# Kernel tuning notes

Hardware: AMD Instinct MI355X
Metric: run time of the kernel (lower is better)

The kernel has to match this reference:

```python
import jax, jax.numpy as jnp
import numpy as np

B, S, D, H = 8, 1500, 1024, 16
HD = D // H
DFF = 4 * D
EPS = 1e-5


def _xavier(key, shape):
    fan_in, fan_out = shape[1], shape[0]
    limit = float(np.sqrt(6.0 / (fan_in + fan_out)))
    return jax.random.uniform(key, shape, jnp.float32, -limit, limit)


def setup_inputs() -> dict:
    key = jax.random.key(0)
    ks = jax.random.split(key, 8)
    return {
        "hidden_states": jax.random.normal(ks[0], (B, S, D), jnp.float32),
        "Wq": _xavier(ks[1], (D, D)),
        "Wk": _xavier(ks[2], (D, D)),
        "Wv": _xavier(ks[3], (D, D)),
        "Wo": _xavier(ks[4], (D, D)),
        "W1": _xavier(ks[5], (DFF, D)),
        "b1": jnp.zeros((DFF,), jnp.float32),
        "W2": _xavier(ks[6], (D, DFF)),
        "b2": jnp.zeros((D,), jnp.float32),
        "ln1_g": jnp.ones((D,), jnp.float32),
        "ln1_b": jnp.zeros((D,), jnp.float32),
        "ln2_g": jnp.ones((D,), jnp.float32),
        "ln2_b": jnp.zeros((D,), jnp.float32),
    }


def _layernorm(x, g, b):
    mu = jnp.mean(x, axis=-1, keepdims=True)
    var = jnp.mean(jnp.square(x - mu), axis=-1, keepdims=True)
    return (x - mu) * jax.lax.rsqrt(var + EPS) * g + b


def reference(hidden_states, Wq, Wk, Wv, Wo, W1, b1, W2, b2, ln1_g, ln1_b, ln2_g, ln2_b):
    x = hidden_states
    residual = x
    h = _layernorm(x, ln1_g, ln1_b)
    # torch Linear: y = h @ W.T ; reshape to heads
    q = (h @ Wq.T).reshape(B, S, H, HD).transpose(0, 2, 1, 3) * (HD ** -0.5)
    k = (h @ Wk.T).reshape(B, S, H, HD).transpose(0, 2, 1, 3)
    v = (h @ Wv.T).reshape(B, S, H, HD).transpose(0, 2, 1, 3)
    scores = jnp.einsum('bhqd,bhkd->bhqk', q, k)
    attn = jax.nn.softmax(scores.astype(jnp.float32), axis=-1).astype(h.dtype)
    ctx = jnp.einsum('bhqk,bhkd->bhqd', attn, v)
    ctx = ctx.transpose(0, 2, 1, 3).reshape(B, S, D)
    x = residual + ctx @ Wo.T
    residual = x
    h = _layernorm(x, ln2_g, ln2_b)
    ffn = jax.nn.gelu(h @ W1.T + b1, approximate=False) @ W2.T + b2
    return residual + ffn
```

## Files before the change

kernel.cpp:

```cpp
#include <hip/hip_runtime.h>
#include <hip/hip_bf16.h>
#include <cstdint>
#include <cstddef>

#define B_    8
#define S_    1500
#define D_    1024
#define H_    16
#define HD_   64
#define DFF_  4096
#define M_    12000
#define VTS_  1536

typedef __bf16 bf16;
typedef __attribute__((ext_vector_type(8))) __bf16 bf16x8;
typedef __attribute__((ext_vector_type(4))) float f32x4;

#define MFMA16(a, b, c) __builtin_amdgcn_mfma_f32_16x16x32_bf16((a), (b), (c), 0, 0, 0)

#define BAR()   do { __builtin_amdgcn_s_barrier(); __builtin_amdgcn_sched_barrier(0); } while (0)

static __device__ __forceinline__ void gload16(const void* g, void* l) {
  __builtin_amdgcn_global_load_lds(
      (const __attribute__((address_space(1))) void*)(uintptr_t)g,
      (__attribute__((address_space(3))) void*)(uintptr_t)l, 16, 0, 0);
}

static __device__ __forceinline__ unsigned short f2bu(float v) {
  bf16 h = (bf16)v;
  union { bf16 h; unsigned short u; } c;
  c.h = h;
  return c.u;
}

static constexpr size_t HSZ      = (size_t)M_ * D_ * 2;
static constexpr size_t H_OFF    = 0;
static constexpr size_t WQ_OFF   = H_OFF + HSZ;
static constexpr size_t WK_OFF   = WQ_OFF + (size_t)D_ * D_ * 2;
static constexpr size_t WV_OFF   = WK_OFF + (size_t)D_ * D_ * 2;
static constexpr size_t WO_OFF   = WV_OFF + (size_t)D_ * D_ * 2;
static constexpr size_t Q_OFF    = WO_OFF + (size_t)D_ * D_ * 2;
static constexpr size_t K_OFF    = Q_OFF + HSZ;
static constexpr size_t VT_OFF   = K_OFF + HSZ;
static constexpr size_t W1_OFF   = VT_OFF + (size_t)128 * 64 * VTS_ * 2;
static constexpr size_t W2_OFF   = W1_OFF + (size_t)DFF_ * D_ * 2;
static constexpr size_t WS_BASE  = W2_OFF + (size_t)DFF_ * D_ * 2;
static constexpr size_t H2B_OFF  = WS_BASE;
static constexpr size_t NEED_BIG = WS_BASE + HSZ;
static constexpr size_t H2F_OFF  = VT_OFF;
static constexpr size_t ACT_OFF  = 0;

__launch_bounds__(256)
__global__ void cvt_bf16(const float* __restrict__ src, bf16* __restrict__ dst, int n) {
  int i = (blockIdx.x * 256 + threadIdx.x) * 4;
  if (i < n) {
    float4 f = *(const float4*)(src + i);
    dst[i + 0] = (bf16)f.x;
    dst[i + 1] = (bf16)f.y;
    dst[i + 2] = (bf16)f.z;
    dst[i + 3] = (bf16)f.w;
  }
}

__launch_bounds__(256)
__global__ void ln_fused(const float* __restrict__ x, const float* __restrict__ g,
                         const float* __restrict__ bb, bf16* __restrict__ out) {
  const int row = blockIdx.x;
  const int t = threadIdx.x;
  const float4 xv = *(const float4*)(x + (size_t)row * D_ + t * 4);
  float s  = xv.x + xv.y + xv.z + xv.w;
  float s2 = xv.x * xv.x + xv.y * xv.y + xv.z * xv.z + xv.w * xv.w;
#pragma unroll
  for (int m = 32; m >= 1; m >>= 1) {
    s  += __shfl_xor(s, m);
    s2 += __shfl_xor(s2, m);
  }
  __shared__ float red[8];
  const int w = t >> 6;
  if ((t & 63) == 0) { red[w] = s; red[4 + w] = s2; }
  __syncthreads();
  s  = red[0] + red[1] + red[2] + red[3];
  s2 = red[4] + red[5] + red[6] + red[7];
  const float mu  = s * (1.0f / D_);
  const float var = s2 * (1.0f / D_) - mu * mu;
  const float rs  = rsqrtf(var + 1e-5f);
  const float4 gv = *(const float4*)(g + t * 4);
  const float4 bv = *(const float4*)(bb + t * 4);
  bf16* o = out + (size_t)row * D_ + t * 4;
  o[0] = (bf16)((xv.x - mu) * rs * gv.x + bv.x);
  o[1] = (bf16)((xv.y - mu) * rs * gv.y + bv.y);
  o[2] = (bf16)((xv.z - mu) * rs * gv.z + bv.z);
  o[3] = (bf16)((xv.w - mu) * rs * gv.w + bv.w);
}

template <int EPI>
__launch_bounds__(512, 2)
__global__ void gemm256(const bf16* __restrict__ A, const bf16* __restrict__ Bw,
                        int M, int N, int K,
                        bf16* __restrict__ outB, float* outF,
                        const float* __restrict__ bias, const float* resid,
                        bf16* __restrict__ outQ, bf16* __restrict__ outK2,
                        bf16* __restrict__ outV) {
  __shared__ bf16 a_lds[4][256 * 32];
  __shared__ bf16 b_lds[4][256 * 32];

  const int t = threadIdx.x;
  const int lane = t & 63, wid = t >> 6;
  const int wm = wid >> 2, wn = wid & 3;
  const int l15 = lane & 15, hi = lane >> 4;
  const int mrow0 = blockIdx.x * 256;
  const int ncol0 = blockIdx.y * 256;

  const int pc = hi ^ ((l15 >> 1) & 3);

  const int s0 = t, s1 = 512 + t;
  const int ar0 = s0 >> 2, ar1 = s1 >> 2;
  const int ac0 = ((s0 & 3) ^ ((ar0 >> 1) & 3)) * 8;
  const int ac1 = ((s1 & 3) ^ ((ar1 >> 1) & 3)) * 8;
  int ga0 = mrow0 + ar0; ga0 = ga0 < M ? ga0 : M - 1;
  int ga1 = mrow0 + ar1; ga1 = ga1 < M ? ga1 : M - 1;
  const bf16* a0 = A + (size_t)ga0 * K + ac0;
  const bf16* a1 = A + (size_t)ga1 * K + ac1;
  const bf16* b0 = Bw + (size_t)(ncol0 + ar0) * K + ac0;
  const bf16* b1 = Bw + (size_t)(ncol0 + ar1) * K + ac1;

  f32x4 acc[8][4] = {};

  const int NT = K >> 5;

#pragma unroll
  for (int pt = 0; pt < 3; ++pt) {
    const int kp = pt << 5;
    gload16(a0 + kp, (char*)&a_lds[pt][0] + s0 * 16);
    gload16(a1 + kp, (char*)&a_lds[pt][0] + s1 * 16);
    gload16(b0 + kp, (char*)&b_lds[pt][0] + s0 * 16);
    gload16(b1 + kp, (char*)&b_lds[pt][0] + s1 * 16);
  }
  asm volatile("s_waitcnt vmcnt(8)" ::: "memory");
  BAR();

  int buf = 0;
  for (int tt = 0; tt < NT; ++tt) {
    const bf16* al = &a_lds[buf][0];
    const bf16* bl = &b_lds[buf][0];
    const bool st3 = (tt + 3) < NT;
    const int nb = (tt + 3) & 3;
    const int k3 = (tt + 3) << 5;

    if (st3) {
      gload16(a0 + k3, (char*)&a_lds[nb][0] + s0 * 16);
      gload16(a1 + k3, (char*)&a_lds[nb][0] + s1 * 16);
      gload16(b0 + k3, (char*)&b_lds[nb][0] + s0 * 16);
      gload16(b1 + k3, (char*)&b_lds[nb][0] + s1 * 16);
    }

    bf16x8 bf_[4], af_[8];
#pragma unroll
    for (int n = 0; n < 4; ++n)
      bf_[n] = *(const bf16x8*)&bl[(wn * 64 + n * 16 + l15) * 32 + pc * 8];
#pragma unroll
    for (int m = 0; m < 8; ++m)
      af_[m] = *(const bf16x8*)&al[(wm * 128 + m * 16 + l15) * 32 + pc * 8];

    __builtin_amdgcn_s_setprio(1);
#pragma unroll
    for (int m = 0; m < 8; ++m)
#pragma unroll
      for (int n = 0; n < 4; ++n)
        acc[m][n] = MFMA16(af_[m], bf_[n], acc[m][n]);
    __builtin_amdgcn_s_setprio(0);

    if (st3)                  asm volatile("s_waitcnt vmcnt(8)" ::: "memory");
    else if ((tt + 2) < NT)   asm volatile("s_waitcnt vmcnt(4)" ::: "memory");
    else                      asm volatile("s_waitcnt vmcnt(0)" ::: "memory");
    BAR();
    buf = (buf + 1) & 3;
  }

  const int r0 = hi * 4;

  if constexpr (EPI == 5) {
    const int mm = blockIdx.y >> 2;
    const int nloc0 = (blockIdx.y & 3) * 256;
    if (mm == 2) {
#pragma unroll
      for (int m = 0; m < 8; ++m) {
        int row0 = mrow0 + wm * 128 + m * 16 + r0;
        if (row0 < M) {
          int bb2 = row0 / 1500;
          int s = row0 - bb2 * 1500;
#pragma unroll
          for (int n = 0; n < 4; ++n) {
            int f = nloc0 + wn * 64 + n * 16 + l15;
            size_t a = ((size_t)(bb2 * 16 + (f >> 6)) * 64 + (f & 63)) * VTS_ + s;
            ushort4 pk;
            pk.x = f2bu(acc[m][n][0]);
            pk.y = f2bu(acc[m][n][1]);
            pk.z = f2bu(acc[m][n][2]);
            pk.w = f2bu(acc[m][n][3]);
            *reinterpret_cast<ushort4*>((unsigned short*)outV + a) = pk;
          }
        }
      }
    } else {
      bf16* dst = (mm == 0) ? outQ : outK2;
      const float sc = (mm == 0) ? 0.18033688011112042f : 1.0f;
#pragma unroll
      for (int m = 0; m < 8; ++m) {
#pragma unroll
        for (int n = 0; n < 4; ++n) {
          int col = nloc0 + wn * 64 + n * 16 + l15;
#pragma unroll
          for (int r = 0; r < 4; ++r) {
            int row = mrow0 + wm * 128 + m * 16 + r0 + r;
            if (row < M) dst[(size_t)row * D_ + col] = (bf16)(acc[m][n][r] * sc);
          }
        }
      }
    }
    return;
  }

#pragma unroll
  for (int m = 0; m < 8; ++m) {
#pragma unroll
    for (int n = 0; n < 4; ++n) {
      int col = ncol0 + wn * 64 + n * 16 + l15;
#pragma unroll
      for (int r = 0; r < 4; ++r) {
        int row = mrow0 + wm * 128 + m * 16 + r0 + r;
        if (row < M) {
          float v = acc[m][n][r];
          if constexpr (EPI == 2) {
            float xg = v + bias[col];
            v = 0.5f * xg * (1.0f + erff(xg * 0.70710678118654752f));
            outB[(size_t)row * N + col] = (bf16)v;
          }
          if constexpr (EPI == 3) {
            v += resid[(size_t)row * N + col];
            if (bias) v += bias[col];
            outF[(size_t)row * N + col] = v;
          }
        }
      }
    }
  }
}

template <int EPI>
__launch_bounds__(256)
__global__ void gemm_bt(const bf16* __restrict__ A, const bf16* __restrict__ Bw,
                        int M, int N, int K,
                        bf16* __restrict__ outB, float* outF,
                        const float* __restrict__ bias, const float* resid,
                        float scale) {
  __shared__ bf16 a_lds[128 * 64];
  __shared__ bf16 b_lds[128 * 64];
  const int t = threadIdx.x;
  const int lane = t & 63, wid = t >> 6;
  const int wr = wid >> 1, wc = wid & 1;
  const int mrow0 = blockIdx.x * 128;
  const int ncol0 = blockIdx.y * 128;
  const int l15 = lane & 15;
  const int khi = (lane >> 4) << 3;

  f32x4 acc[4][4] = {};

  for (int k0 = 0; k0 < K; k0 += 64) {
#pragma unroll
    for (int i = 0; i < 4; ++i) {
      int idx = i * 2048 + t * 8;
      int row = idx >> 6, col = idx & 63;
      int gr = mrow0 + row;
      gr = gr < M ? gr : M - 1;
      gload16(A + (size_t)gr * K + (k0 + col), (char*)a_lds + idx * 2);
    }
#pragma unroll
    for (int i = 0; i < 4; ++i) {
      int idx = i * 2048 + t * 8;
      int row = idx >> 6, col = idx & 63;
      gload16(Bw + (size_t)(ncol0 + row) * K + (k0 + col), (char*)b_lds + idx * 2);
    }
    __syncthreads();
#pragma unroll
    for (int kk = 0; kk < 2; ++kk) {
      bf16x8 af[4], bfv[4];
#pragma unroll
      for (int m = 0; m < 4; ++m)
        af[m] = *(const bf16x8*)&a_lds[(wr * 64 + m * 16 + l15) * 64 + kk * 32 + khi];
#pragma unroll
      for (int n = 0; n < 4; ++n)
        bfv[n] = *(const bf16x8*)&b_lds[(wc * 64 + n * 16 + l15) * 64 + kk * 32 + khi];
#pragma unroll
      for (int m = 0; m < 4; ++m)
#pragma unroll
        for (int n = 0; n < 4; ++n)
          acc[m][n] = MFMA16(af[m], bfv[n], acc[m][n]);
    }
    __syncthreads();
  }

  const int r0 = (lane >> 4) << 2;
#pragma unroll
  for (int m = 0; m < 4; ++m) {
#pragma unroll
    for (int n = 0; n < 4; ++n) {
      int col = ncol0 + wc * 64 + n * 16 + l15;
#pragma unroll
      for (int r = 0; r < 4; ++r) {
        int row = mrow0 + wr * 64 + m * 16 + r0 + r;
        if (row < M) {
          float v = acc[m][n][r];
          if constexpr (EPI == 2) {
            float xg = v + bias[col];
            v = 0.5f * xg * (1.0f + erff(xg * 0.70710678118654752f));
          }
          if constexpr (EPI == 3) {
            v += resid[(size_t)row * N + col];
            if (bias) v += bias[col];
            outF[(size_t)row * N + col] = v;
          } else {
            outB[(size_t)row * N + col] = (bf16)v;
          }
        }
      }
    }
  }
}

__launch_bounds__(256, 4)
__global__ void attn_fwd6(const bf16* __restrict__ q, const bf16* __restrict__ kg,
                          const bf16* __restrict__ vt, bf16* __restrict__ cx) {
  __shared__ bf16 k_lds[2][64 * 64];
  __shared__ bf16 v_lds[2][64 * 64];
  __shared__ bf16 p_lds[4][16 * 64];

  const int t = threadIdx.x;
  const int lane = t & 63, w = t >> 6;
  const int L = blockIdx.x;
  const int wu = (L & 7) * 384 + (L >> 3);
  const int bh = wu / 24;
  const int qt = wu - bh * 24;
  const int l15 = lane & 15;
  const int hi = lane >> 4;
  const int khi = hi << 3;

  const size_t hoff = ((size_t)(bh >> 4) * S_) * D_ + (size_t)(bh & 15) * HD_;
  const bf16* qh = q + hoff;
  const bf16* kh = kg + hoff;
  const bf16* vh = vt + (size_t)bh * (64 * VTS_);

  const int st_r0 = t >> 3;
  const int st_c  = t & 7;

  int qr = qt * 64 + w * 16 + l15;
  int qrc = qr < S_ ? qr : S_ - 1;
  const bf16x8 qf0 = *(const bf16x8*)(qh + (size_t)qrc * D_ + khi);
  const bf16x8 qf1 = *(const bf16x8*)(qh + (size_t)qrc * D_ + 32 + khi);

  f32x4 oacc[4] = {};
  float mrun[4], lrun[4];
#pragma unroll
  for (int r = 0; r < 4; ++r) { mrun[r] = -1e30f; lrun[r] = 0.f; }

  bf16* pw = &p_lds[w][0];
  const int NT = (S_ + 63) / 64;
  const float THR = 11.5415605f;

#pragma unroll
  for (int i = 0; i < 2; ++i) {
    int row = i * 32 + st_r0;
    int sc = st_c ^ (row & 7);
    int key = row < S_ ? row : S_ - 1;
    gload16(kh + (size_t)key * D_ + sc * 8, (char*)&k_lds[0][0] + (i * 2048 + t * 8) * 2);
    gload16(vh + (size_t)row * VTS_ + sc * 8, (char*)&v_lds[0][0] + (i * 2048 + t * 8) * 2);
  }
  __syncthreads();

  int buf = 0;
  for (int kt = 0; kt < NT; ++kt) {
    if (kt + 1 < NT) {
      int kb = (kt + 1) * 64;
#pragma unroll
      for (int i = 0; i < 2; ++i) {
        int row = i * 32 + st_r0;
        int sc = st_c ^ (row & 7);
        int key = kb + row;
        key = key < S_ ? key : S_ - 1;
        gload16(kh + (size_t)key * D_ + sc * 8,
                (char*)&k_lds[buf ^ 1][0] + (i * 2048 + t * 8) * 2);
        gload16(vh + (size_t)row * VTS_ + kb + sc * 8,
                (char*)&v_lds[buf ^ 1][0] + (i * 2048 + t * 8) * 2);
      }
    }

    float pv[4][4];
    __builtin_amdgcn_s_setprio(1);
#pragma unroll
    for (int nb = 0; nb < 4; ++nb) {
      int krow = nb * 16 + l15;
      f32x4 z = {};
      z = MFMA16(qf0, *(const bf16x8*)&k_lds[buf][krow * 64 + ((hi ^ (l15 & 7)) << 3)], z);
      z = MFMA16(qf1, *(const bf16x8*)&k_lds[buf][krow * 64 + (((4 + hi) ^ (l15 & 7)) << 3)], z);
#pragma unroll
      for (int r = 0; r < 4; ++r) pv[nb][r] = z[r];
    }
    __builtin_amdgcn_s_setprio(0);

    if (kt == NT - 1) {
#pragma unroll
      for (int nb = 0; nb < 4; ++nb) {
        bool cvld = (kt * 64 + nb * 16 + l15) < S_;
#pragma unroll
        for (int r = 0; r < 4; ++r) pv[nb][r] = cvld ? pv[nb][r] : -1e30f;
      }
    }

    float lmax[4];
    bool ok = true;
#pragma unroll
    for (int r = 0; r < 4; ++r) {
      lmax[r] = fmaxf(fmaxf(pv[0][r], pv[1][r]), fmaxf(pv[2][r], pv[3][r]));
      ok = ok && (lmax[r] <= mrun[r] + THR);
    }
    if (!__all(ok)) {
#pragma unroll
      for (int r = 0; r < 4; ++r) {
        float mx = lmax[r];
        mx = fmaxf(mx, __shfl_xor(mx, 1));
        mx = fmaxf(mx, __shfl_xor(mx, 2));
        mx = fmaxf(mx, __shfl_xor(mx, 4));
        mx = fmaxf(mx, __shfl_xor(mx, 8));
        float mnew = fmaxf(mrun[r], mx);
        float corr = exp2f(mrun[r] - mnew);
        lrun[r] *= corr;
        mrun[r] = mnew;
#pragma unroll
        for (int db = 0; db < 4; ++db) oacc[db][r] *= corr;
      }
    }

#pragma unroll
    for (int r = 0; r < 4; ++r) {
      float p0 = exp2f(pv[0][r] - mrun[r]);
      float p1 = exp2f(pv[1][r] - mrun[r]);
      float p2 = exp2f(pv[2][r] - mrun[r]);
      float p3 = exp2f(pv[3][r] - mrun[r]);
      pv[0][r] = p0; pv[1][r] = p1; pv[2][r] = p2; pv[3][r] = p3;
      lrun[r] += (p0 + p1) + (p2 + p3);
    }

#pragma unroll
    for (int nb = 0; nb < 4; ++nb) {
#pragma unroll
      for (int r = 0; r < 4; ++r) {
        int prow = hi * 4 + r;
        int pcol = (nb * 16 + l15) ^ ((prow & 7) << 3);
        pw[prow * 64 + pcol] = (bf16)pv[nb][r];
      }
    }

    __builtin_amdgcn_s_setprio(1);
#pragma unroll
    for (int kk = 0; kk < 2; ++kk) {
      bf16x8 pf = *(const bf16x8*)&pw[l15 * 64 + (((kk * 4 + hi) ^ (l15 & 7)) << 3)];
#pragma unroll
      for (int db = 0; db < 4; ++db) {
        int vrow = db * 16 + l15;
        bf16x8 vf = *(const bf16x8*)&v_lds[buf][vrow * 64 + (((kk * 4 + hi) ^ (l15 & 7)) << 3)];
        oacc[db] = MFMA16(pf, vf, oacc[db]);
      }
    }
    __builtin_amdgcn_s_setprio(0);

    __syncthreads();
    buf ^= 1;
  }

#pragma unroll
  for (int r = 0; r < 4; ++r) {
    float ps = lrun[r];
    ps += __shfl_xor(ps, 1);
    ps += __shfl_xor(ps, 2);
    ps += __shfl_xor(ps, 4);
    ps += __shfl_xor(ps, 8);
    int qrow = qt * 64 + w * 16 + hi * 4 + r;
    if (qrow < S_) {
      float inv = 1.0f / ps;
#pragma unroll
      for (int db = 0; db < 4; ++db)
        cx[hoff + (size_t)qrow * D_ + db * 16 + l15] = (bf16)(oacc[db][r] * inv);
    }
  }
}

extern "C" void kernel_launch(void* const* d_in, const int* in_sizes, int n_in,
                              void* d_out, int out_size, void* d_ws, size_t ws_size,
                              hipStream_t stream) {
  const float* x   = (const float*)d_in[0];
  const float* Wq  = (const float*)d_in[1];
  const float* Wk  = (const float*)d_in[2];
  const float* Wv  = (const float*)d_in[3];
  const float* Wo  = (const float*)d_in[4];
  const float* W1  = (const float*)d_in[5];
  const float* b1  = (const float*)d_in[6];
  const float* W2  = (const float*)d_in[7];
  const float* b2  = (const float*)d_in[8];
  const float* g1  = (const float*)d_in[9];
  const float* be1 = (const float*)d_in[10];
  const float* g2  = (const float*)d_in[11];
  const float* be2 = (const float*)d_in[12];
  float* out = (float*)d_out;

  char* ws = (char*)d_ws;
  bf16* h_b   = (bf16*)(ws + H_OFF);
  bf16* wq_b  = (bf16*)(ws + WQ_OFF);
  bf16* wk_b  = (bf16*)(ws + WK_OFF);
  bf16* wv_b  = (bf16*)(ws + WV_OFF);
  bf16* wo_b  = (bf16*)(ws + WO_OFF);
  bf16* w1_b  = (bf16*)(ws + W1_OFF);
  bf16* w2_b  = (bf16*)(ws + W2_OFF);
  bf16* q_b   = (bf16*)(ws + Q_OFF);
  bf16* k_b   = (bf16*)(ws + K_OFF);
  bf16* vt_b  = (bf16*)(ws + VT_OFF);
  bf16* act_b = (bf16*)(ws + ACT_OFF);
  bf16* ctx_b = h_b;

  const bool big = ws_size >= NEED_BIG;
  bf16* h2_b = (bf16*)(ws + (big ? H2B_OFF : H2F_OFF));

  cvt_bf16<<<(D_ * D_) / 1024, 256, 0, stream>>>(Wq, wq_b, D_ * D_);
  cvt_bf16<<<(D_ * D_) / 1024, 256, 0, stream>>>(Wk, wk_b, D_ * D_);
  cvt_bf16<<<(D_ * D_) / 1024, 256, 0, stream>>>(Wv, wv_b, D_ * D_);
  cvt_bf16<<<(D_ * D_) / 1024, 256, 0, stream>>>(Wo, wo_b, D_ * D_);
  cvt_bf16<<<(DFF_ * D_) / 1024, 256, 0, stream>>>(W1, w1_b, DFF_ * D_);
  cvt_bf16<<<(DFF_ * D_) / 1024, 256, 0, stream>>>(W2, w2_b, DFF_ * D_);

  ln_fused<<<M_, 256, 0, stream>>>(x, g1, be1, h_b);

  gemm256<5><<<dim3((M_ + 255) / 256, 12), 512, 0, stream>>>(
      h_b, wq_b, M_, 3072, D_, nullptr, nullptr, nullptr, nullptr, q_b, k_b, vt_b);

  attn_fwd6<<<3072, 256, 0, stream>>>(q_b, k_b, vt_b, ctx_b);

  gemm256<3><<<dim3((M_ + 255) / 256, 4), 512, 0, stream>>>(
      ctx_b, wo_b, M_, D_, D_, nullptr, out, nullptr, x, nullptr, nullptr, nullptr);

  ln_fused<<<M_, 256, 0, stream>>>(out, g2, be2, h2_b);

  if (big) {
    gemm256<2><<<dim3((M_ + 255) / 256, DFF_ / 256), 512, 0, stream>>>(
        h2_b, w1_b, M_, DFF_, D_, act_b, nullptr, b1, nullptr,
        nullptr, nullptr, nullptr);
    gemm256<3><<<dim3((M_ + 255) / 256, D_ / 256), 512, 0, stream>>>(
        act_b, w2_b, M_, D_, DFF_, nullptr, out, b2, out,
        nullptr, nullptr, nullptr);
  } else {
    for (int c = 0; c < 3; ++c) {
      int r0c = c * 4000;
      int nr = 4000;
      gemm256<2><<<dim3((nr + 255) / 256, DFF_ / 256), 512, 0, stream>>>(
          h2_b + (size_t)r0c * D_, w1_b, nr, DFF_, D_, act_b, nullptr, b1, nullptr,
          nullptr, nullptr, nullptr);
      gemm_bt<3><<<dim3((nr + 127) / 128, D_ / 128), 256, 0, stream>>>(
          act_b, w2_b, nr, D_, DFF_, nullptr, out + (size_t)r0c * D_, b2,
          out + (size_t)r0c * D_, 0.f);
    }
  }
}
```

Baseline: 728.6 us.

## Restructure 256x256 GEMM to 1024 threads, K=64 double-buffered LDS tiles

The GEMM kernel goes from 512 to 1024 threads per block. Each of the 16 waves now computes a 64x64 sub-tile instead of 128x64, and the K-step grows from 32 to 64. The 4-stage pipeline with 32-wide K slices is replaced by a 2-stage double buffer with a new XOR swizzle and __syncthreads barriers. This cuts per-thread accumulator registers and adds waves to hide latency, at the cost of a shallower prefetch depth and a full barrier every K step.

```diff
diff --git a/kernel.cpp b/kernel.cpp
--- a/kernel.cpp
+++ b/kernel.cpp
@@ -17,8 +17,6 @@
 typedef __attribute__((ext_vector_type(4))) float f32x4;
 
 #define MFMA16(a, b, c) __builtin_amdgcn_mfma_f32_16x16x32_bf16((a), (b), (c), 0, 0, 0)
-
-#define BAR()   do { __builtin_amdgcn_s_barrier(); __builtin_amdgcn_sched_barrier(0); } while (0)
 
 static __device__ __forceinline__ void gload16(const void* g, void* l) {
   __builtin_amdgcn_global_load_lds(
@@ -94,87 +92,83 @@
 }
 
 template <int EPI>
-__launch_bounds__(512, 2)
+__launch_bounds__(1024, 4)
 __global__ void gemm256(const bf16* __restrict__ A, const bf16* __restrict__ Bw,
                         int M, int N, int K,
                         bf16* __restrict__ outB, float* outF,
                         const float* __restrict__ bias, const float* resid,
                         bf16* __restrict__ outQ, bf16* __restrict__ outK2,
                         bf16* __restrict__ outV) {
-  __shared__ bf16 a_lds[4][256 * 32];
-  __shared__ bf16 b_lds[4][256 * 32];
+  __shared__ bf16 a_lds[2][256 * 64];
+  __shared__ bf16 b_lds[2][256 * 64];
 
   const int t = threadIdx.x;
   const int lane = t & 63, wid = t >> 6;
   const int wm = wid >> 2, wn = wid & 3;
   const int l15 = lane & 15, hi = lane >> 4;
+  const int l7 = l15 & 7;
   const int mrow0 = blockIdx.x * 256;
   const int ncol0 = blockIdx.y * 256;
 
-  const int pc = hi ^ ((l15 >> 1) & 3);
-
-  const int s0 = t, s1 = 512 + t;
-  const int ar0 = s0 >> 2, ar1 = s1 >> 2;
-  const int ac0 = ((s0 & 3) ^ ((ar0 >> 1) & 3)) * 8;
-  const int ac1 = ((s1 & 3) ^ ((ar1 >> 1) & 3)) * 8;
-  int ga0 = mrow0 + ar0; ga0 = ga0 < M ? ga0 : M - 1;
-  int ga1 = mrow0 + ar1; ga1 = ga1 < M ? ga1 : M - 1;
-  const bf16* a0 = A + (size_t)ga0 * K + ac0;
-  const bf16* a1 = A + (size_t)ga1 * K + ac1;
-  const bf16* b0 = Bw + (size_t)(ncol0 + ar0) * K + ac0;
-  const bf16* b1 = Bw + (size_t)(ncol0 + ar1) * K + ac1;
-
-  f32x4 acc[8][4] = {};
-
-  const int NT = K >> 5;
-
-#pragma unroll
-  for (int pt = 0; pt < 3; ++pt) {
-    const int kp = pt << 5;
-    gload16(a0 + kp, (char*)&a_lds[pt][0] + s0 * 16);
-    gload16(a1 + kp, (char*)&a_lds[pt][0] + s1 * 16);
-    gload16(b0 + kp, (char*)&b_lds[pt][0] + s0 * 16);
-    gload16(b1 + kp, (char*)&b_lds[pt][0] + s1 * 16);
-  }
-  asm volatile("s_waitcnt vmcnt(8)" ::: "memory");
-  BAR();
+  const int rl = t >> 3;
+  const int sc8 = ((t & 7) ^ (rl & 7)) << 3;
+  unsigned offA[2], offB[2];
+#pragma unroll
+  for (int j = 0; j < 2; ++j) {
+    int gr = mrow0 + j * 128 + rl; gr = gr < M ? gr : M - 1;
+    offA[j] = (unsigned)gr * (unsigned)K + (unsigned)sc8;
+    offB[j] = (unsigned)(ncol0 + j * 128 + rl) * (unsigned)K + (unsigned)sc8;
+  }
+
+  f32x4 acc[4][4] = {};
+
+  const int NT = K >> 6;
+
+  {
+    char* ad = (char*)&a_lds[0][0];
+    char* bd = (char*)&b_lds[0][0];
+    gload16(A + offA[0], ad + t * 16);
+    gload16(A + offA[1], ad + 16384 + t * 16);
+    gload16(Bw + offB[0], bd + t * 16);
+    gload16(Bw + offB[1], bd + 16384 + t * 16);
+  }
+  __syncthreads();
 
   int buf = 0;
   for (int tt = 0; tt < NT; ++tt) {
+    if (tt + 1 < NT) {
+      const unsigned k1 = (unsigned)(tt + 1) << 6;
+      char* ad = (char*)&a_lds[buf ^ 1][0];
+      char* bd = (char*)&b_lds[buf ^ 1][0];
+      gload16(A + offA[0] + k1, ad + t * 16);
+      gload16(A + offA[1] + k1, ad + 16384 + t * 16);
+      gload16(Bw + offB[0] + k1, bd + t * 16);
+      gload16(Bw + offB[1] + k1, bd + 16384 + t * 16);
+    }
+
     const bf16* al = &a_lds[buf][0];
     const bf16* bl = &b_lds[buf][0];
-    const bool st3 = (tt + 3) < NT;
-    const int nb = (tt + 3) & 3;
-    const int k3 = (tt + 3) << 5;
-
-    if (st3) {
-      gload16(a0 + k3, (char*)&a_lds[nb][0] + s0 * 16);
-      gload16(a1 + k3, (char*)&a_lds[nb][0] + s1 * 16);
-      gload16(b0 + k3, (char*)&b_lds[nb][0] + s0 * 16);
-      gload16(b1 + k3, (char*)&b_lds[nb][0] + s1 * 16);
-    }
-
-    bf16x8 bf_[4], af_[8];
-#pragma unroll
-    for (int n = 0; n < 4; ++n)
-      bf_[n] = *(const bf16x8*)&bl[(wn * 64 + n * 16 + l15) * 32 + pc * 8];
-#pragma unroll
-    for (int m = 0; m < 8; ++m)
-      af_[m] = *(const bf16x8*)&al[(wm * 128 + m * 16 + l15) * 32 + pc * 8];
-
-    __builtin_amdgcn_s_setprio(1);
-#pragma unroll
-    for (int m = 0; m < 8; ++m)
+#pragma unroll
+    for (int kk = 0; kk < 2; ++kk) {
+      bf16x8 af_[4], bf_[4];
+      const int cc = ((kk * 4 + hi) ^ l7) << 3;
+#pragma unroll
+      for (int m = 0; m < 4; ++m)
+        af_[m] = *(const bf16x8*)&al[(wm * 64 + m * 16 + l15) * 64 + cc];
 #pragma unroll
       for (int n = 0; n < 4; ++n)
-        acc[m][n] = MFMA16(af_[m], bf_[n], acc[m][n]);
-    __builtin_amdgcn_s_setprio(0);
-
-    if (st3)                  asm volatile("s_waitcnt vmcnt(8)" ::: "memory");
-    else if ((tt + 2) < NT)   asm volatile("s_waitcnt vmcnt(4)" ::: "memory");
-    else                      asm volatile("s_waitcnt vmcnt(0)" ::: "memory");
-    BAR();
-    buf = (buf + 1) & 3;
+        bf_[n] = *(const bf16x8*)&bl[(wn * 64 + n * 16 + l15) * 64 + cc];
+      __builtin_amdgcn_s_setprio(1);
+#pragma unroll
+      for (int m = 0; m < 4; ++m)
+#pragma unroll
+        for (int n = 0; n < 4; ++n)
+          acc[m][n] = MFMA16(af_[m], bf_[n], acc[m][n]);
+      __builtin_amdgcn_s_setprio(0);
+    }
+
+    __syncthreads();
+    buf ^= 1;
   }
 
   const int r0 = hi * 4;
@@ -184,8 +178,8 @@
     const int nloc0 = (blockIdx.y & 3) * 256;
     if (mm == 2) {
 #pragma unroll
-      for (int m = 0; m < 8; ++m) {
-        int row0 = mrow0 + wm * 128 + m * 16 + r0;
+      for (int m = 0; m < 4; ++m) {
+        int row0 = mrow0 + wm * 64 + m * 16 + r0;
         if (row0 < M) {
           int bb2 = row0 / 1500;
           int s = row0 - bb2 * 1500;
@@ -206,13 +200,13 @@
       bf16* dst = (mm == 0) ? outQ : outK2;
       const float sc = (mm == 0) ? 0.18033688011112042f : 1.0f;
 #pragma unroll
-      for (int m = 0; m < 8; ++m) {
+      for (int m = 0; m < 4; ++m) {
 #pragma unroll
         for (int n = 0; n < 4; ++n) {
           int col = nloc0 + wn * 64 + n * 16 + l15;
 #pragma unroll
           for (int r = 0; r < 4; ++r) {
-            int row = mrow0 + wm * 128 + m * 16 + r0 + r;
+            int row = mrow0 + wm * 64 + m * 16 + r0 + r;
             if (row < M) dst[(size_t)row * D_ + col] = (bf16)(acc[m][n][r] * sc);
           }
         }
@@ -222,13 +216,13 @@
   }
 
 #pragma unroll
-  for (int m = 0; m < 8; ++m) {
+  for (int m = 0; m < 4; ++m) {
 #pragma unroll
     for (int n = 0; n < 4; ++n) {
       int col = ncol0 + wn * 64 + n * 16 + l15;
 #pragma unroll
       for (int r = 0; r < 4; ++r) {
-        int row = mrow0 + wm * 128 + m * 16 + r0 + r;
+        int row = mrow0 + wm * 64 + m * 16 + r0 + r;
         if (row < M) {
           float v = acc[m][n][r];
           if constexpr (EPI == 2) {
@@ -538,28 +532,28 @@
 
   ln_fused<<<M_, 256, 0, stream>>>(x, g1, be1, h_b);
 
-  gemm256<5><<<dim3((M_ + 255) / 256, 12), 512, 0, stream>>>(
+  gemm256<5><<<dim3((M_ + 255) / 256, 12), 1024, 0, stream>>>(
       h_b, wq_b, M_, 3072, D_, nullptr, nullptr, nullptr, nullptr, q_b, k_b, vt_b);
 
   attn_fwd6<<<3072, 256, 0, stream>>>(q_b, k_b, vt_b, ctx_b);
 
-  gemm256<3><<<dim3((M_ + 255) / 256, 4), 512, 0, stream>>>(
+  gemm256<3><<<dim3((M_ + 255) / 256, 4), 1024, 0, stream>>>(
       ctx_b, wo_b, M_, D_, D_, nullptr, out, nullptr, x, nullptr, nullptr, nullptr);
 
   ln_fused<<<M_, 256, 0, stream>>>(out, g2, be2, h2_b);
 
   if (big) {
-    gemm256<2><<<dim3((M_ + 255) / 256, DFF_ / 256), 512, 0, stream>>>(
+    gemm256<2><<<dim3((M_ + 255) / 256, DFF_ / 256), 1024, 0, stream>>>(
         h2_b, w1_b, M_, DFF_, D_, act_b, nullptr, b1, nullptr,
         nullptr, nullptr, nullptr);
-    gemm256<3><<<dim3((M_ + 255) / 256, D_ / 256), 512, 0, stream>>>(
+    gemm256<3><<<dim3((M_ + 255) / 256, D_ / 256), 1024, 0, stream>>>(
         act_b, w2_b, M_, D_, DFF_, nullptr, out, b2, out,
         nullptr, nullptr, nullptr);
   } else {
     for (int c = 0; c < 3; ++c) {
       int r0c = c * 4000;
       int nr = 4000;
-      gemm256<2><<<dim3((nr + 255) / 256, DFF_ / 256), 512, 0, stream>>>(
+      gemm256<2><<<dim3((nr + 255) / 256, DFF_ / 256), 1024, 0, stream>>>(
           h2_b + (size_t)r0c * D_, w1_b, nr, DFF_, D_, act_b, nullptr, b1, nullptr,
           nullptr, nullptr, nullptr);
       gemm_bt<3><<<dim3((nr + 127) / 128, D_ / 128), 256, 0, stream>>>(
```

Measured after the change: 643.3 us. 11.7% less time.
